# Kernel tuning notes

Hardware: AMD Instinct MI355X
Metric: run time of the kernel (lower is better)

The kernel has to match this reference:

```python
import jax, jax.numpy as jnp
import numpy as np
from jax.scipy.special import gammaln

NEARZERO = 1e-5
LENF = 15  # gamma unit-hydrograph length (days)

# (name, low, high) in the exact order of Exphydro.parameter_bounds
PHY_BOUNDS = [
    ('ddf', 0.0, 40.0), ('Tbm', -2.0, 3.0), ('wrf', 0.0, 0.5), ('Tbf', -5.0, 2.0),
    ('Kf', 0.0, 5.0), ('exp_fe', 0.0, 1.0), ('ET_efficiency', 0.0, 1.0),
    ('coef_runoff', 0.0, 1.0), ('coef_vadose2phreatic', 1e-5, 0.02),
    ('coef_vadose', 0.0, 0.1), ('coef_phreatic', 1e-5, 0.01),
    ('vadose_max_level', 1e-3, 500.0)]
ROUT_BOUNDS = [('alpha1', 0.3, 20.0), ('beta1', 0.01, 5.0),
               ('alpha2', 0.5, 13.0), ('beta2', 0.15, 1.5)]


def setup_inputs() -> dict:
    key = jax.random.key(0)
    k1, k2, k3, k4 = jax.random.split(key, 4)
    T, G = 1095, 15000
    prcp = jax.random.uniform(k1, (T, G), dtype=jnp.float32) * 10.0   # mm/day
    tmean = jax.random.normal(k2, (T, G), dtype=jnp.float32) * 10.0   # deg C (spans <0 and >0)
    pet = jax.random.uniform(k3, (T, G), dtype=jnp.float32) * 5.0     # mm/day
    x_phy = jnp.stack([prcp, tmean, pet], axis=-1)                    # [T, G, 3]
    params = jax.random.uniform(k4, (G, 16), dtype=jnp.float32)       # normalized in [0,1]
    return {'x_phy': x_phy, 'params': params}


def _descale(p, lo, hi):
    # change_param_range: linear rescale of [0,1]-normalized params
    return p * (hi - lo) + lo


def _uh_gamma(alpha, theta, lenF=LENF):
    # Gamma-pdf unit hydrograph, normalized. alpha, theta: [G] -> w: [lenF, G]
    t = jnp.arange(lenF, dtype=alpha.dtype) + 0.5          # midpoint of each day
    a = alpha[None, :]
    th = theta[None, :]
    logw = (a - 1.0) * jnp.log(t[:, None]) - t[:, None] / th - gammaln(a) - a * jnp.log(th)
    w = jnp.exp(logw)
    return w / jnp.sum(w, axis=0, keepdims=True)


def _uh_conv(q, w):
    # causal depthwise convolution along time. q: [T, G], w: [L, G]
    T = q.shape[0]
    L = w.shape[0]
    qp = jnp.pad(q, ((L - 1, 0), (0, 0)))
    out = jnp.zeros_like(q)
    for l in range(L):  # fixed small L=15, unrolled at trace time
        out = out + w[l][None, :] * qp[L - 1 - l:L - 1 - l + T]
    return out


def _forward(x_phy, params):
    G = params.shape[0]
    # unpack + descale: 12 static physical params [G,1] (nmul=1), 4 routing params [G]
    phy = {name: _descale(params[:, i:i + 1], lo, hi)
           for i, (name, lo, hi) in enumerate(PHY_BOUNDS)}
    rout = {name: _descale(params[:, 12 + i], lo, hi)
            for i, (name, lo, hi) in enumerate(ROUT_BOUNDS)}

    P = x_phy[..., 0:1]    # [T, G, 1] precip
    Tm = x_phy[..., 1:2]   # [T, G, 1] mean temperature
    Pet = x_phy[..., 2:3]  # [T, G, 1] potential ET

    def step(carry, inp):
        sog, wis, vad, phr = carry  # snow-on-ground, water-in-snowpack, vadose, phreatic [G,1]
        p, tm, pet = inp
        rain = p * (tm >= 0.0).astype(p.dtype)
        snow = p * (tm < 0.0).astype(p.dtype)
        # overnight refreezing of liquid water in snowpack
        pot_freeze = phy['Kf'] * jnp.clip(phy['Tbf'] - tm, NEARZERO, None) ** phy['exp_fe']
        freeze = jnp.minimum(pot_freeze, wis)
        wis = wis - freeze
        sog = sog + freeze
        # degree-day snowmelt
        melt = jnp.minimum(jnp.clip(phy['ddf'] * (tm - phy['Tbm']), 0.0, None), sog + snow)
        sog = sog + snow - melt
        # snowpack liquid retention
        retention = phy['wrf'] * sog
        wtmp = wis + melt + rain
        avail = jnp.clip(wtmp - retention, 0.0, None)
        wis = jnp.where(avail > 0.0, retention, wtmp)
        # soil buckets
        ret_pot = phy['ET_efficiency'] * pet
        ratio = vad / phy['vadose_max_level']
        ht0 = phy['coef_runoff'] * ratio * avail                 # surface runoff
        infil = avail - ht0
        ht1 = phy['coef_vadose2phreatic'] * ratio * vad          # vadose -> phreatic
        ht2 = phy['coef_vadose'] * vad                           # delayed runoff (interflow)
        ht3 = phy['coef_phreatic'] * phr                         # baseflow
        aet = jnp.minimum(ret_pot, vad)                          # actual ET
        vad = vad + infil - aet - ht1 - ht2
        overflow = jnp.clip(vad - phy['vadose_max_level'], 0.0, None)
        vad = jnp.clip(vad, NEARZERO, phy['vadose_max_level'])
        ht0 = ht0 + overflow
        phr = jnp.clip(phr + ht1 - ht3, NEARZERO, None)
        return (sog, wis, vad, phr), (ht0, ht2, ht3, aet, vad, phr)

    init = tuple(jnp.full((G, 1), NEARZERO, dtype=x_phy.dtype) for _ in range(4))
    _, (ht0, ht2, ht3, aet, vad_sim, phr_sim) = jax.lax.scan(step, init, (P, Tm, Pet))

    # average over nmul (muwts=None, nmul=1) -> [T, G]
    q_surf = jnp.mean(ht0, axis=-1)
    q_delay = jnp.mean(ht2 + ht3, axis=-1)
    # gamma unit-hydrograph routing
    uh1 = _uh_gamma(rout['alpha1'], rout['beta1'])
    uh2 = _uh_gamma(rout['alpha2'], rout['beta2'])
    return _uh_conv(q_surf, uh1) + _uh_conv(q_delay, uh2)  # streamflow [T, G]


def reference(x_phy, params):
    return _forward(x_phy, params)
```

## Files before the change

kernel.cpp:

```cpp
#include <hip/hip_runtime.h>

#define LENF 15
#define NZ   1e-5f

typedef float f32x2 __attribute__((ext_vector_type(2)));

struct R3 { float p, t, e; };

__global__ __launch_bounds__(64, 1) void exphydro_kernel(
    const float* __restrict__ x,
    const float* __restrict__ params,
    float* __restrict__ out,
    int G, int T)
{
  int g = blockIdx.x * 64 + threadIdx.x;
  if (g >= G) return;

  const float* pp = params + (size_t)g * 16;
  float P0[16];
#pragma unroll
  for (int i = 0; i < 16; ++i) P0[i] = pp[i];

  const float ddf    = P0[0]  * 40.f;
  const float Tbm    = P0[1]  * 5.f  - 2.f;
  const float wrf    = P0[2]  * 0.5f;
  const float Tbf    = P0[3]  * 7.f  - 5.f;
  const float Kf     = P0[4]  * 5.f;
  const float exp_fe = P0[5];
  const float ET_eff = P0[6];
  const float c_run  = P0[7];
  const float c_v2p  = P0[8]  * (0.02f - 1e-5f) + 1e-5f;
  const float c_vad  = P0[9]  * 0.1f;
  const float c_phr  = P0[10] * (0.01f - 1e-5f) + 1e-5f;
  const float vml    = P0[11] * (500.f - 0.001f) + 0.001f;
  const float a1     = P0[12] * (20.f - 0.3f)  + 0.3f;
  const float b1     = P0[13] * (5.f  - 0.01f) + 0.01f;
  const float a2     = P0[14] * (13.f - 0.5f)  + 0.5f;
  const float b2     = P0[15] * (1.5f - 0.15f) + 0.15f;
  const float inv_vml = 1.f / vml;

  f32x2 wv[LENF];
  {
    float lw1[LENF], lw2[LENF];
    float m1 = -1e30f, m2 = -1e30f;
    const float ib1 = 1.f / b1, ib2 = 1.f / b2;
#pragma unroll
    for (int l = 0; l < LENF; ++l) {
      float tt = l + 0.5f;
      float lt = __logf(tt);
      lw1[l] = (a1 - 1.f) * lt - tt * ib1;
      lw2[l] = (a2 - 1.f) * lt - tt * ib2;
      m1 = fmaxf(m1, lw1[l]);
      m2 = fmaxf(m2, lw2[l]);
    }
    float s1 = 0.f, s2 = 0.f;
    float t1[LENF], t2[LENF];
#pragma unroll
    for (int l = 0; l < LENF; ++l) {
      t1[l] = __expf(lw1[l] - m1); s1 += t1[l];
      t2[l] = __expf(lw2[l] - m2); s2 += t2[l];
    }
    const float r1 = 1.f / s1, r2 = 1.f / s2;
#pragma unroll
    for (int l = 0; l < LENF; ++l) { wv[l].x = t1[l] * r1; wv[l].y = t2[l] * r2; }
  }

  float sog = NZ, wis = NZ, vad = NZ, phr = NZ;
  f32x2 acc[LENF];
#pragma unroll
  for (int l = 0; l < LENF; ++l) { acc[l].x = 0.f; acc[l].y = 0.f; }

  const unsigned Gu = (unsigned)G;
  const R3* xg = (const R3*)x + g;
  float* optr = out + g;

  R3 A[LENF], B[LENF];
  float pf[LENF], mp[LENF], rn[LENF], sn[LENF], rp[LENF];

  const int nb   = T / LENF;
  const int tail = T - nb * LENF;

#define LOAD(BUF, blk)                                                \
  {                                                                   \
    unsigned b0_ = (unsigned)(blk) * (unsigned)(LENF) * Gu;           \
    _Pragma("unroll")                                                 \
    for (int j = 0; j < LENF; ++j) BUF[j] = xg[b0_ + (unsigned)j * Gu];\
  }

#define LOAD_G(BUF, blk)                                              \
  {                                                                   \
    unsigned b0_ = (unsigned)(blk) * (unsigned)(LENF) * Gu;           \
    _Pragma("unroll")                                                 \
    for (int j = 0; j < LENF; ++j) {                                  \
      if ((blk) * LENF + j < T) BUF[j] = xg[b0_ + (unsigned)j * Gu];  \
      else { BUF[j].p = 0.f; BUF[j].t = 0.f; BUF[j].e = 0.f; }        \
    }                                                                 \
  }

#define PREP(BUF)                                                     \
  {                                                                   \
    _Pragma("unroll")                                                 \
    for (int j = 0; j < LENF; ++j) {                                  \
      float p_ = BUF[j].p, tm_ = BUF[j].t, pe_ = BUF[j].e;            \
      float r_ = (tm_ >= 0.f) ? p_ : 0.f;                             \
      rn[j] = r_;                                                     \
      sn[j] = p_ - r_;                                                \
      pf[j] = Kf * __builtin_amdgcn_exp2f(                            \
                  exp_fe * __builtin_amdgcn_logf(fmaxf(Tbf - tm_, NZ))); \
      mp[j] = fmaxf(ddf * (tm_ - Tbm), 0.f);                          \
      rp[j] = ET_eff * pe_;                                           \
    }                                                                 \
  }

#define STEP(I_)                                                      \
  {                                                                   \
    float freeze = fminf(pf[I_], wis);                                \
    wis -= freeze;                                                    \
    float sos = sog + freeze + sn[I_];                                \
    float melt = fminf(mp[I_], sos);                                  \
    sog = sos - melt;                                                 \
    float retention = wrf * sog;                                      \
    float wtmp = wis + melt + rn[I_];                                 \
    float avail = fmaxf(wtmp - retention, 0.f);                       \
    wis = fminf(wtmp, retention);  \
    float ratio = vad * inv_vml;                                      \
    float ht0 = c_run * ratio * avail;                                \
    float infil = avail - ht0;                                        \
    float ht1 = c_v2p * ratio * vad;                                  \
    float ht2 = c_vad * vad;                                          \
    float ht3 = c_phr * phr;                                          \
    float aet = fminf(rp[I_], vad);                                   \
    vad = vad + infil - aet - ht1 - ht2;                              \
    float overflow = fmaxf(vad - vml, 0.f);                           \
    vad = fminf(fmaxf(vad, NZ), vml);                                 \
    ht0 += overflow;                                                  \
    phr = fmaxf(phr + ht1 - ht3, NZ);                                 \
    f32x2 q_; q_.x = ht0; q_.y = ht2 + ht3;                           \
    _Pragma("unroll")                                                 \
    for (int l = 0; l < LENF; ++l) {                                  \
      int s_ = (I_) + l; if (s_ >= LENF) s_ -= LENF;                  \
      acc[s_] += wv[l] * q_;              \
    }                                                                 \
  }

#define BLOCK()                                                       \
  {                                                                   \
    _Pragma("unroll")                                                 \
    for (int i = 0; i < LENF; ++i) {                                  \
      STEP(i);                                                        \
      f32x2 a_ = acc[i];                                              \
      *optr = a_.x + a_.y;                                            \
      acc[i].x = 0.f; acc[i].y = 0.f;                                 \
      optr += G;                                                      \
    }                                                                 \
  }

#define BLOCK_G(t0)                                                   \
  {                                                                   \
    _Pragma("unroll")                                                 \
    for (int i = 0; i < LENF; ++i) {                                  \
      if ((t0) + i < T) {                                             \
        STEP(i);                                                      \
        f32x2 a_ = acc[i];                                            \
        *optr = a_.x + a_.y;                                          \
        acc[i].x = 0.f; acc[i].y = 0.f;                               \
        optr += G;                                                    \
      }                                                               \
    }                                                                 \
  }

  if (nb > 0) LOAD(A, 0);

  int k = 0;
  while (k + 2 <= nb) {
    LOAD(B, k + 1);
    PREP(A);
    BLOCK();
    if (k + 2 < nb) LOAD(A, k + 2);
    PREP(B);
    BLOCK();
    k += 2;
  }
  if (k < nb) {
    PREP(A);
    BLOCK();
  }
  if (tail > 0) {
    LOAD_G(A, nb);
    PREP(A);
    BLOCK_G(nb * LENF);
  }

#undef LOAD
#undef LOAD_G
#undef PREP
#undef STEP
#undef BLOCK
#undef BLOCK_G
}

extern "C" void kernel_launch(void* const* d_in, const int* in_sizes, int n_in,
                              void* d_out, int out_size, void* d_ws, size_t ws_size,
                              hipStream_t stream) {
  const float* x      = (const float*)d_in[0];
  const float* params = (const float*)d_in[1];
  float* out          = (float*)d_out;

  int G = in_sizes[1] / 16;
  int T = in_sizes[0] / (G * 3);

  int block = 64;
  int grid  = (G + block - 1) / block;
  exphydro_kernel<<<grid, block, 0, stream>>>(x, params, out, G, T);
}
```

Baseline: 149.8 us.

## Process two catchments per thread to interleave independent recurrences

Each thread now simulates two grid cells (g and g+half) and interleaves their serial time-step recurrences, so one cell's latency chain can hide the other's. The grid is halved to 118 blocks of 64 threads, which on a 256-CU device leaves many CUs idle. The PREP batching of transcendental work is folded into the step, and the rotating accumulator writes its last slot directly instead of zeroing it. Register pressure roughly doubles, so spills are a risk.

Result: slower. 377.1 us (+151.7%).

```diff
diff --git a/kernel.cpp b/kernel.cpp
--- a/kernel.cpp
+++ b/kernel.cpp
@@ -6,6 +6,106 @@
 typedef float f32x2 __attribute__((ext_vector_type(2)));
 
 struct R3 { float p, t, e; };
+
+struct Cell {
+  float ddf, Tbm, wrf, Tbf, Kf, exp_fe, ET_eff, c_run, c_v2p, c_vad, c_phr,
+        vml, inv_vml;
+  float sog, wis, vad, phr;
+  f32x2 wv[LENF];
+  f32x2 acc[LENF];
+};
+
+__device__ __forceinline__ void init_cell(Cell& c, const float* pp) {
+  float P0[16];
+#pragma unroll
+  for (int i = 0; i < 16; ++i) P0[i] = pp[i];
+  c.ddf    = P0[0]  * 40.f;
+  c.Tbm    = P0[1]  * 5.f  - 2.f;
+  c.wrf    = P0[2]  * 0.5f;
+  c.Tbf    = P0[3]  * 7.f  - 5.f;
+  c.Kf     = P0[4]  * 5.f;
+  c.exp_fe = P0[5];
+  c.ET_eff = P0[6];
+  c.c_run  = P0[7];
+  c.c_v2p  = P0[8]  * (0.02f - 1e-5f) + 1e-5f;
+  c.c_vad  = P0[9]  * 0.1f;
+  c.c_phr  = P0[10] * (0.01f - 1e-5f) + 1e-5f;
+  c.vml    = P0[11] * (500.f - 0.001f) + 0.001f;
+  c.inv_vml = 1.f / c.vml;
+  const float a1 = P0[12] * (20.f - 0.3f)  + 0.3f;
+  const float b1 = P0[13] * (5.f  - 0.01f) + 0.01f;
+  const float a2 = P0[14] * (13.f - 0.5f)  + 0.5f;
+  const float b2 = P0[15] * (1.5f - 0.15f) + 0.15f;
+
+  float lw1[LENF], lw2[LENF];
+  float m1 = -1e30f, m2 = -1e30f;
+  const float ib1 = 1.f / b1, ib2 = 1.f / b2;
+#pragma unroll
+  for (int l = 0; l < LENF; ++l) {
+    float tt = l + 0.5f;
+    float lt = __logf(tt);
+    lw1[l] = (a1 - 1.f) * lt - tt * ib1;
+    lw2[l] = (a2 - 1.f) * lt - tt * ib2;
+    m1 = fmaxf(m1, lw1[l]);
+    m2 = fmaxf(m2, lw2[l]);
+  }
+  float s1 = 0.f, s2 = 0.f;
+  float t1[LENF], t2[LENF];
+#pragma unroll
+  for (int l = 0; l < LENF; ++l) {
+    t1[l] = __expf(lw1[l] - m1); s1 += t1[l];
+    t2[l] = __expf(lw2[l] - m2); s2 += t2[l];
+  }
+  const float r1 = 1.f / s1, r2 = 1.f / s2;
+#pragma unroll
+  for (int l = 0; l < LENF; ++l) { c.wv[l].x = t1[l] * r1; c.wv[l].y = t2[l] * r2; }
+
+  c.sog = NZ; c.wis = NZ; c.vad = NZ; c.phr = NZ;
+#pragma unroll
+  for (int l = 0; l < LENF; ++l) { c.acc[l].x = 0.f; c.acc[l].y = 0.f; }
+}
+
+__device__ __forceinline__ float step_cell(Cell& c, R3 r, int i) {
+  float p = r.p, tm = r.t, pe = r.e;
+  float rain = (tm >= 0.f) ? p : 0.f;
+  float snow = p - rain;
+  float pot_freeze = c.Kf * __builtin_amdgcn_exp2f(
+      c.exp_fe * __builtin_amdgcn_logf(fmaxf(c.Tbf - tm, NZ)));
+  float freeze = fminf(pot_freeze, c.wis);
+  c.wis -= freeze;
+  float sos = c.sog + freeze + snow;
+  float melt = fminf(fmaxf(c.ddf * (tm - c.Tbm), 0.f), sos);
+  c.sog = sos - melt;
+  float retention = c.wrf * c.sog;
+  float wtmp = c.wis + melt + rain;
+  float avail = fmaxf(wtmp - retention, 0.f);
+  c.wis = fminf(wtmp, retention);
+  float ratio = c.vad * c.inv_vml;
+  float ht0 = c.c_run * ratio * avail;
+  float infil = avail - ht0;
+  float ht1 = c.c_v2p * ratio * c.vad;
+  float ht2 = c.c_vad * c.vad;
+  float ht3 = c.c_phr * c.phr;
+  float aet = fminf(c.ET_eff * pe, c.vad);
+  c.vad = c.vad + infil - aet - ht1 - ht2;
+  float overflow = fmaxf(c.vad - c.vml, 0.f);
+  c.vad = fminf(fmaxf(c.vad, NZ), c.vml);
+  ht0 += overflow;
+  c.phr = fmaxf(c.phr + ht1 - ht3, NZ);
+
+  f32x2 q; q.x = ht0; q.y = ht2 + ht3;
+  f32x2 ov = c.acc[i] + c.wv[0] * q;
+#pragma unroll
+  for (int l = 1; l < LENF - 1; ++l) {
+    int s = i + l; if (s >= LENF) s -= LENF;
+    c.acc[s] += c.wv[l] * q;
+  }
+  {
+    int s = i + LENF - 1; if (s >= LENF) s -= LENF;
+    c.acc[s] = c.wv[LENF - 1] * q;
+  }
+  return ov.x + ov.y;
+}
 
 __global__ __launch_bounds__(64, 1) void exphydro_kernel(
     const float* __restrict__ x,
@@ -13,190 +113,93 @@
     float* __restrict__ out,
     int G, int T)
 {
+  const int half = (G + 1) >> 1;
   int g = blockIdx.x * 64 + threadIdx.x;
-  if (g >= G) return;
-
-  const float* pp = params + (size_t)g * 16;
-  float P0[16];
-#pragma unroll
-  for (int i = 0; i < 16; ++i) P0[i] = pp[i];
-
-  const float ddf    = P0[0]  * 40.f;
-  const float Tbm    = P0[1]  * 5.f  - 2.f;
-  const float wrf    = P0[2]  * 0.5f;
-  const float Tbf    = P0[3]  * 7.f  - 5.f;
-  const float Kf     = P0[4]  * 5.f;
-  const float exp_fe = P0[5];
-  const float ET_eff = P0[6];
-  const float c_run  = P0[7];
-  const float c_v2p  = P0[8]  * (0.02f - 1e-5f) + 1e-5f;
-  const float c_vad  = P0[9]  * 0.1f;
-  const float c_phr  = P0[10] * (0.01f - 1e-5f) + 1e-5f;
-  const float vml    = P0[11] * (500.f - 0.001f) + 0.001f;
-  const float a1     = P0[12] * (20.f - 0.3f)  + 0.3f;
-  const float b1     = P0[13] * (5.f  - 0.01f) + 0.01f;
-  const float a2     = P0[14] * (13.f - 0.5f)  + 0.5f;
-  const float b2     = P0[15] * (1.5f - 0.15f) + 0.15f;
-  const float inv_vml = 1.f / vml;
-
-  f32x2 wv[LENF];
-  {
-    float lw1[LENF], lw2[LENF];
-    float m1 = -1e30f, m2 = -1e30f;
-    const float ib1 = 1.f / b1, ib2 = 1.f / b2;
-#pragma unroll
-    for (int l = 0; l < LENF; ++l) {
-      float tt = l + 0.5f;
-      float lt = __logf(tt);
-      lw1[l] = (a1 - 1.f) * lt - tt * ib1;
-      lw2[l] = (a2 - 1.f) * lt - tt * ib2;
-      m1 = fmaxf(m1, lw1[l]);
-      m2 = fmaxf(m2, lw2[l]);
-    }
-    float s1 = 0.f, s2 = 0.f;
-    float t1[LENF], t2[LENF];
-#pragma unroll
-    for (int l = 0; l < LENF; ++l) {
-      t1[l] = __expf(lw1[l] - m1); s1 += t1[l];
-      t2[l] = __expf(lw2[l] - m2); s2 += t2[l];
-    }
-    const float r1 = 1.f / s1, r2 = 1.f / s2;
-#pragma unroll
-    for (int l = 0; l < LENF; ++l) { wv[l].x = t1[l] * r1; wv[l].y = t2[l] * r2; }
-  }
-
-  float sog = NZ, wis = NZ, vad = NZ, phr = NZ;
-  f32x2 acc[LENF];
-#pragma unroll
-  for (int l = 0; l < LENF; ++l) { acc[l].x = 0.f; acc[l].y = 0.f; }
+  if (g >= half) return;
+  const int g2 = g + half;
+  const bool hasY = (g2 < G);
+  const int g2s = hasY ? g2 : (G - 1);
+
+  Cell cx, cy;
+  init_cell(cx, params + (size_t)g * 16);
+  init_cell(cy, params + (size_t)g2s * 16);
 
   const unsigned Gu = (unsigned)G;
-  const R3* xg = (const R3*)x + g;
-  float* optr = out + g;
-
-  R3 A[LENF], B[LENF];
-  float pf[LENF], mp[LENF], rn[LENF], sn[LENF], rp[LENF];
+  const R3* xgx = (const R3*)x + g;
+  const R3* xgy = (const R3*)x + g2s;
+  float* ox = out + g;
+  float* oy = out + g2s;
+
+  R3 AX[LENF], BX[LENF], AY[LENF], BY[LENF];
 
   const int nb   = T / LENF;
   const int tail = T - nb * LENF;
 
-#define LOAD(BUF, blk)                                                \
-  {                                                                   \
-    unsigned b0_ = (unsigned)(blk) * (unsigned)(LENF) * Gu;           \
-    _Pragma("unroll")                                                 \
-    for (int j = 0; j < LENF; ++j) BUF[j] = xg[b0_ + (unsigned)j * Gu];\
-  }
-
-#define LOAD_G(BUF, blk)                                              \
-  {                                                                   \
-    unsigned b0_ = (unsigned)(blk) * (unsigned)(LENF) * Gu;           \
+#define LOAD(BUF, XG, blk)                                            \
+  {                                                                   \
+    unsigned b0_ = (unsigned)(blk) * (unsigned)LENF * Gu;             \
+    _Pragma("unroll")                                                 \
+    for (int j = 0; j < LENF; ++j) BUF[j] = (XG)[b0_ + (unsigned)j * Gu]; \
+  }
+
+#define LOAD_G(BUF, XG, blk)                                          \
+  {                                                                   \
+    unsigned b0_ = (unsigned)(blk) * (unsigned)LENF * Gu;             \
     _Pragma("unroll")                                                 \
     for (int j = 0; j < LENF; ++j) {                                  \
-      if ((blk) * LENF + j < T) BUF[j] = xg[b0_ + (unsigned)j * Gu];  \
+      if ((blk) * LENF + j < T) BUF[j] = (XG)[b0_ + (unsigned)j * Gu];\
       else { BUF[j].p = 0.f; BUF[j].t = 0.f; BUF[j].e = 0.f; }        \
     }                                                                 \
   }
 
-#define PREP(BUF)                                                     \
-  {                                                                   \
-    _Pragma("unroll")                                                 \
-    for (int j = 0; j < LENF; ++j) {                                  \
-      float p_ = BUF[j].p, tm_ = BUF[j].t, pe_ = BUF[j].e;            \
-      float r_ = (tm_ >= 0.f) ? p_ : 0.f;                             \
-      rn[j] = r_;                                                     \
-      sn[j] = p_ - r_;                                                \
-      pf[j] = Kf * __builtin_amdgcn_exp2f(                            \
-                  exp_fe * __builtin_amdgcn_logf(fmaxf(Tbf - tm_, NZ))); \
-      mp[j] = fmaxf(ddf * (tm_ - Tbm), 0.f);                          \
-      rp[j] = ET_eff * pe_;                                           \
+#define PAIR_BLOCK(BUFX, BUFY)                                        \
+  {                                                                   \
+    _Pragma("unroll")                                                 \
+    for (int i = 0; i < LENF; ++i) {                                  \
+      float vx = step_cell(cx, BUFX[i], i);                           \
+      float vy = step_cell(cy, BUFY[i], i);                           \
+      *ox = vx;                                                       \
+      if (hasY) *oy = vy;                                             \
+      ox += G; oy += G;                                               \
     }                                                                 \
   }
 
-#define STEP(I_)                                                      \
-  {                                                                   \
-    float freeze = fminf(pf[I_], wis);                                \
-    wis -= freeze;                                                    \
-    float sos = sog + freeze + sn[I_];                                \
-    float melt = fminf(mp[I_], sos);                                  \
-    sog = sos - melt;                                                 \
-    float retention = wrf * sog;                                      \
-    float wtmp = wis + melt + rn[I_];                                 \
-    float avail = fmaxf(wtmp - retention, 0.f);                       \
-    wis = fminf(wtmp, retention);  \
-    float ratio = vad * inv_vml;                                      \
-    float ht0 = c_run * ratio * avail;                                \
-    float infil = avail - ht0;                                        \
-    float ht1 = c_v2p * ratio * vad;                                  \
-    float ht2 = c_vad * vad;                                          \
-    float ht3 = c_phr * phr;                                          \
-    float aet = fminf(rp[I_], vad);                                   \
-    vad = vad + infil - aet - ht1 - ht2;                              \
-    float overflow = fmaxf(vad - vml, 0.f);                           \
-    vad = fminf(fmaxf(vad, NZ), vml);                                 \
-    ht0 += overflow;                                                  \
-    phr = fmaxf(phr + ht1 - ht3, NZ);                                 \
-    f32x2 q_; q_.x = ht0; q_.y = ht2 + ht3;                           \
-    _Pragma("unroll")                                                 \
-    for (int l = 0; l < LENF; ++l) {                                  \
-      int s_ = (I_) + l; if (s_ >= LENF) s_ -= LENF;                  \
-      acc[s_] += wv[l] * q_;              \
-    }                                                                 \
-  }
-
-#define BLOCK()                                                       \
-  {                                                                   \
-    _Pragma("unroll")                                                 \
-    for (int i = 0; i < LENF; ++i) {                                  \
-      STEP(i);                                                        \
-      f32x2 a_ = acc[i];                                              \
-      *optr = a_.x + a_.y;                                            \
-      acc[i].x = 0.f; acc[i].y = 0.f;                                 \
-      optr += G;                                                      \
-    }                                                                 \
-  }
-
-#define BLOCK_G(t0)                                                   \
+#define PAIR_BLOCK_G(BUFX, BUFY, t0)                                  \
   {                                                                   \
     _Pragma("unroll")                                                 \
     for (int i = 0; i < LENF; ++i) {                                  \
       if ((t0) + i < T) {                                             \
-        STEP(i);                                                      \
-        f32x2 a_ = acc[i];                                            \
-        *optr = a_.x + a_.y;                                          \
-        acc[i].x = 0.f; acc[i].y = 0.f;                               \
-        optr += G;                                                    \
+        float vx = step_cell(cx, BUFX[i], i);                         \
+        float vy = step_cell(cy, BUFY[i], i);                         \
+        *ox = vx;                                                     \
+        if (hasY) *oy = vy;                                           \
+        ox += G; oy += G;                                             \
       }                                                               \
     }                                                                 \
   }
 
-  if (nb > 0) LOAD(A, 0);
+  if (nb > 0) { LOAD(AX, xgx, 0); LOAD(AY, xgy, 0); }
 
   int k = 0;
   while (k + 2 <= nb) {
-    LOAD(B, k + 1);
-    PREP(A);
-    BLOCK();
-    if (k + 2 < nb) LOAD(A, k + 2);
-    PREP(B);
-    BLOCK();
+    LOAD(BX, xgx, k + 1); LOAD(BY, xgy, k + 1);
+    PAIR_BLOCK(AX, AY);
+    if (k + 2 < nb) { LOAD(AX, xgx, k + 2); LOAD(AY, xgy, k + 2); }
+    PAIR_BLOCK(BX, BY);
     k += 2;
   }
   if (k < nb) {
-    PREP(A);
-    BLOCK();
+    PAIR_BLOCK(AX, AY);
   }
   if (tail > 0) {
-    LOAD_G(A, nb);
-    PREP(A);
-    BLOCK_G(nb * LENF);
+    LOAD_G(AX, xgx, nb); LOAD_G(AY, xgy, nb);
+    PAIR_BLOCK_G(AX, AY, nb * LENF);
   }
 
 #undef LOAD
 #undef LOAD_G
-#undef PREP
-#undef STEP
-#undef BLOCK
-#undef BLOCK_G
+#undef PAIR_BLOCK
+#undef PAIR_BLOCK_G
 }
 
 extern "C" void kernel_launch(void* const* d_in, const int* in_sizes, int n_in,
@@ -209,7 +212,8 @@
   int G = in_sizes[1] / 16;
   int T = in_sizes[0] / (G * 3);
 
+  int half  = (G + 1) / 2;
   int block = 64;
-  int grid  = (G + block - 1) / block;
+  int grid  = (half + block - 1) / block;
   exphydro_kernel<<<grid, block, 0, stream>>>(x, params, out, G, T);
 }
```
